# Kernel tuning notes

Measured on AMD Instinct MI355X. Metric: run time of the kernel, lower is better.

## Reference

```python
import jax, jax.numpy as jnp
import numpy as np

EMB = 768
HEADS = 8
WS = 14  # window size


def setup_inputs() -> dict:
    key = jax.random.key(0)
    k1, k2, k3 = jax.random.split(key, 3)
    B, N, C = 16, 3136, EMB
    x = jax.random.normal(k1, (B, N, C), dtype=jnp.float32)
    s = 1.0 / np.sqrt(C)
    w_qkv = jax.random.normal(k2, (C, 3 * C), dtype=jnp.float32) * s
    b_qkv = jnp.zeros((3 * C,), dtype=jnp.float32)
    w_proj = jax.random.normal(k3, (C, C), dtype=jnp.float32) * s
    b_proj = jnp.zeros((C,), dtype=jnp.float32)
    return {"x": x, "w_qkv": w_qkv, "b_qkv": b_qkv, "w_proj": w_proj, "b_proj": b_proj}


def _window_partition(x, ws):
    # (B, H, W, C) -> (B*nWin, ws*ws, C)
    B, H, W, C = x.shape
    x = x.reshape(B, H // ws, ws, W // ws, ws, C)
    x = x.transpose(0, 1, 3, 2, 4, 5)
    return x.reshape(-1, ws * ws, C)


def _window_reverse(windows, H, W, ws):
    # (B*nWin, ws*ws, C) -> (B, H, W, C)
    C = windows.shape[-1]
    B = windows.shape[0] // ((H // ws) * (W // ws))
    x = windows.reshape(B, H // ws, W // ws, ws, ws, C)
    x = x.transpose(0, 1, 3, 2, 4, 5)
    return x.reshape(B, H, W, C)


def reference(x, w_qkv, b_qkv, w_proj, b_proj):
    B, N, C = x.shape
    H = W = int(np.sqrt(N))
    nh, d = HEADS, C // HEADS
    x4 = x.reshape(B, H, W, C)
    shortcut = x  # residual in (B, N, C) layout

    xw = _window_partition(x4, WS)  # (nb, n, C), n = WS*WS
    nb, n, _ = xw.shape

    qkv = xw @ w_qkv + b_qkv  # (nb, n, 3C)
    # einops 'b n (h d qkv)': qkv index varies fastest within last dim
    qkv = qkv.reshape(nb, n, nh, d, 3)
    qkv = jnp.transpose(qkv, (4, 0, 2, 1, 3))  # (3, nb, h, n, d)
    q, k, v = qkv[0], qkv[1], qkv[2]

    energy = jnp.einsum('bhqd,bhkd->bhqk', q, k)
    # NOTE: faithful to source — softmax FIRST, then divide by sqrt(emb_size)
    att = jax.nn.softmax(energy, axis=-1) / jnp.sqrt(jnp.float32(C))
    out = jnp.einsum('bhqk,bhkd->bhqd', att, v)
    out = out.transpose(0, 2, 1, 3).reshape(nb, n, C)  # (nb, n, h*d)
    out = out @ w_proj + b_proj

    out = _window_reverse(out, H, W, WS).reshape(B, N, C)
    return out + shortcut
```

## Files before the change

### kernel.cpp

```cpp
#include <hip/hip_runtime.h>


#define NWIN 256
#define NTOK 196
#define CDIM 768
#define NHEAD 8
#define DHEAD 96
#define C3 2304

typedef unsigned short u16;
typedef unsigned int u32;
typedef __attribute__((ext_vector_type(8))) short bf16x8;
typedef __attribute__((ext_vector_type(4))) float f32x4;

__device__ __forceinline__ float bf2f(u16 u) {
    union { u32 i; float f; } cv;
    cv.i = ((u32)u) << 16;
    return cv.f;
}
__device__ __forceinline__ float2 bfp2f(u32 u) {
    union { u32 i; float f; } lo, hi;
    lo.i = u << 16;
    hi.i = u & 0xFFFF0000u;
    float2 r; r.x = lo.f; r.y = hi.f;
    return r;
}
__device__ __forceinline__ u16 f2bf(float f) {
    union { float f; u32 i; } cv;
    cv.f = f;
    u32 x = cv.i;
    x = x + 0x7FFFu + ((x >> 16) & 1u);
    return (u16)(x >> 16);
}
__device__ __forceinline__ u32 pack2bf(float a, float b) {
    return (u32)f2bf(a) | ((u32)f2bf(b) << 16);
}

__global__ void detect_kernel(const u16* __restrict__ w, int* __restrict__ flag) {
    __shared__ int any;
    int t = threadIdx.x;
    if (t == 0) any = 0;
    __syncthreads();
    int hit = 0;
    for (int i = 0; i < 16; ++i) {
        u16 u = w[t * 16 + i];
        int e = (u >> 7) & 0xFF;
        if (e >= 140) hit = 1;
    }
    if (hit) atomicOr(&any, 1);
    __syncthreads();
    if (t == 0) flag[0] = any;
}

template<bool FP32>
__global__ __launch_bounds__(256, 2) void qkvmm_kernel(
    const void* __restrict__ xv, const void* __restrict__ wqv,
    const void* __restrict__ bvv, const int* __restrict__ flag,
    u16* __restrict__ qb, u16* __restrict__ kb, u16* __restrict__ vb,
    int win0, int mtiles)
{
    if (flag[0] != (FP32 ? 1 : 0)) return;
    __shared__ u16 As[128 * 40];
    __shared__ u16 Bs[192 * 40];

    int t = threadIdx.x;
    int mb = blockIdx.x % mtiles;
    int nb = blockIdx.x / mtiles;

    int arow = t >> 1, ahalf = t & 1;
    int rloc = mb * 128 + arow;
    int wiL = rloc / 196, tok = rloc - wiL * 196;
    int wiA = win0 + wiL;
    int b_ = wiA >> 4, wrem = wiA & 15, wr = wrem >> 2, wc = wrem & 3;
    int tr = tok / 14, tc = tok - tr * 14;
    size_t xrow = ((size_t)b_ * 3136 + (size_t)((wr * 14 + tr) * 56 + wc * 14 + tc)) * CDIM;

    int kp = t >> 4, dg = t & 15;
    int d0 = nb * 64 + dg * 4;
    int hB = d0 / 96, dh0 = d0 - hB * 96;
    int sb = hB * 288 + 3 * dh0;

    f32x4 acc[4][6];
#pragma unroll
    for (int m = 0; m < 4; ++m)
#pragma unroll
        for (int n = 0; n < 6; ++n)
            acc[m][n] = (f32x4){0.f, 0.f, 0.f, 0.f};

    int lane = t & 63, wvid = t >> 6;
    int wm = wvid >> 1, wn = wvid & 1;
    int lo = lane & 15, hi = lane >> 4;

#pragma unroll 1
    for (int kk = 0; kk < 24; ++kk) {
        int k0 = kk * 32;
        {
            u32* dst = (u32*)&As[arow * 40 + ahalf * 16];
            if (FP32) {
                const float4* xp = (const float4*)((const float*)xv + xrow + k0 + ahalf * 16);
                float4 f0 = xp[0], f1 = xp[1], f2 = xp[2], f3 = xp[3];
                dst[0] = pack2bf(f0.x, f0.y); dst[1] = pack2bf(f0.z, f0.w);
                dst[2] = pack2bf(f1.x, f1.y); dst[3] = pack2bf(f1.z, f1.w);
                dst[4] = pack2bf(f2.x, f2.y); dst[5] = pack2bf(f2.z, f2.w);
                dst[6] = pack2bf(f3.x, f3.y); dst[7] = pack2bf(f3.z, f3.w);
            } else {
                const uint4* xp = (const uint4*)((const u16*)xv + xrow + k0 + ahalf * 16);
                ((uint4*)dst)[0] = xp[0];
                ((uint4*)dst)[1] = xp[1];
            }
        }
        if (FP32) {
            const float* w0p = (const float*)wqv + (size_t)(k0 + 2 * kp) * C3 + sb;
            const float* w1p = w0p + C3;
#pragma unroll
            for (int e = 0; e < 12; ++e) {
                int c = (e % 3) * 64 + dg * 4 + e / 3;
                *(u32*)&Bs[c * 40 + 2 * kp] = pack2bf(w0p[e], w1p[e]);
            }
        } else {
            const u16* w0p = (const u16*)wqv + (size_t)(k0 + 2 * kp) * C3 + sb;
            const u16* w1p = w0p + C3;
#pragma unroll
            for (int e = 0; e < 12; ++e) {
                int c = (e % 3) * 64 + dg * 4 + e / 3;
                *(u32*)&Bs[c * 40 + 2 * kp] = (u32)w0p[e] | ((u32)w1p[e] << 16);
            }
        }
        __syncthreads();
        bf16x8 af[4], bfr[6];
#pragma unroll
        for (int m = 0; m < 4; ++m)
            af[m] = *(const bf16x8*)&As[(wm * 64 + m * 16 + lo) * 40 + hi * 8];
#pragma unroll
        for (int n = 0; n < 6; ++n)
            bfr[n] = *(const bf16x8*)&Bs[(wn * 96 + n * 16 + lo) * 40 + hi * 8];
#pragma unroll
        for (int m = 0; m < 4; ++m)
#pragma unroll
            for (int n = 0; n < 6; ++n)
                acc[m][n] = __builtin_amdgcn_mfma_f32_16x16x32_bf16(af[m], bfr[n], acc[m][n], 0, 0, 0);
        __syncthreads();
    }

    float bias[6];
    int h2_[6], dh2_[6], wh_[6];
#pragma unroll
    for (int n = 0; n < 6; ++n) {
        int c = wn * 96 + n * 16 + lo;
        wh_[n] = c >> 6;
        int d_abs = nb * 64 + (c & 63);
        h2_[n] = d_abs / 96; dh2_[n] = d_abs - h2_[n] * 96;
        int bcol = h2_[n] * 288 + 3 * dh2_[n] + wh_[n];
        bias[n] = FP32 ? ((const float*)bvv)[bcol] : bf2f(((const u16*)bvv)[bcol]);
    }
#pragma unroll
    for (int m = 0; m < 4; ++m) {
#pragma unroll
        for (int j = 0; j < 4; ++j) {
            int rr = mb * 128 + wm * 64 + m * 16 + hi * 4 + j;
            int wir = rr / 196, tk = rr - wir * 196;
            size_t rowpart = (size_t)wir * (8 * 196) + (size_t)tk;
#pragma unroll
            for (int n = 0; n < 6; ++n) {
                u16* ob = wh_[n] == 0 ? qb : (wh_[n] == 1 ? kb : vb);
                ob[(rowpart + (size_t)h2_[n] * 196) * 96 + dh2_[n]] =
                    f2bf(acc[m][n][j] + bias[n]);
            }
        }
    }
}

template<bool FP32>
__global__ __launch_bounds__(256, 2) void attn_kernel(
    const u16* __restrict__ qbp, const u16* __restrict__ kbp,
    const u16* __restrict__ vbp, u16* __restrict__ ao,
    const int* __restrict__ flag, int win0)
{
    if (flag[0] != (FP32 ? 1 : 0)) return;
    __shared__ u16 Vt[96 * 232];
    __shared__ u16 Pl[4 * 16 * 232];

    int bh = blockIdx.x;
    int t  = threadIdx.x;
    int lane = t & 63, w = t >> 6;
    int lo = lane & 15, hi = lane >> 4;

    const u16* qbase = qbp + (size_t)bh * (NTOK * DHEAD);
    const u16* kbase = kbp + (size_t)bh * (NTOK * DHEAD);
    const u16* vbase = vbp + (size_t)bh * (NTOK * DHEAD);
    u16* obase = ao + ((size_t)bh + (size_t)win0 * 8) * (NTOK * DHEAD);

#pragma unroll 1
    for (int i = t; i < 112 * 12; i += 256) {
        int tp = i % 112, dgv = i / 112;
        int dbase = dgv * 8, cpos = 2 * tp;
        uint4 a = {0, 0, 0, 0}, bq = {0, 0, 0, 0};
        if (tp < 98) {
            const u16* v0 = vbase + (size_t)(2 * tp) * 96 + dbase;
            a  = *(const uint4*)v0;
            bq = *(const uint4*)(v0 + 96);
        }
        *(u32*)&Vt[(dbase + 0) * 232 + cpos] = (a.x & 0xFFFFu) | (bq.x << 16);
        *(u32*)&Vt[(dbase + 1) * 232 + cpos] = (a.x >> 16) | (bq.x & 0xFFFF0000u);
        *(u32*)&Vt[(dbase + 2) * 232 + cpos] = (a.y & 0xFFFFu) | (bq.y << 16);
        *(u32*)&Vt[(dbase + 3) * 232 + cpos] = (a.y >> 16) | (bq.y & 0xFFFF0000u);
        *(u32*)&Vt[(dbase + 4) * 232 + cpos] = (a.z & 0xFFFFu) | (bq.z << 16);
        *(u32*)&Vt[(dbase + 5) * 232 + cpos] = (a.z >> 16) | (bq.z & 0xFFFF0000u);
        *(u32*)&Vt[(dbase + 6) * 232 + cpos] = (a.w & 0xFFFFu) | (bq.w << 16);
        *(u32*)&Vt[(dbase + 7) * 232 + cpos] = (a.w >> 16) | (bq.w & 0xFFFF0000u);
    }
    __syncthreads();

    u16* pw = Pl + w * (16 * 232);
#pragma unroll 1
    for (int i = 0; i < 4; ++i) {
        int qt = w + 4 * i;
        if (qt >= 13) break;
        int qrow = qt * 16 + lo; if (qrow > 195) qrow = 195;
        bf16x8 qf[3];
#pragma unroll
        for (int ks = 0; ks < 3; ++ks)
            qf[ks] = *(const bf16x8*)(qbase + (size_t)qrow * 96 + ks * 32 + hi * 8);
        f32x4 sc[13];
#pragma unroll
        for (int kt = 0; kt < 13; ++kt) sc[kt] = (f32x4){0.f, 0.f, 0.f, 0.f};
#pragma unroll
        for (int kt = 0; kt < 13; ++kt) {
            int krow = kt * 16 + lo; if (krow > 195) krow = 195;
            const u16* kr = kbase + (size_t)krow * 96;
#pragma unroll
            for (int ks = 0; ks < 3; ++ks) {
                bf16x8 kf = *(const bf16x8*)(kr + ks * 32 + hi * 8);
                sc[kt] = __builtin_amdgcn_mfma_f32_16x16x32_bf16(kf, qf[ks], sc[kt], 0, 0, 0);
            }
        }
        float p[52];
        float mx = -1e30f;
#pragma unroll
        for (int kt = 0; kt < 13; ++kt)
#pragma unroll
            for (int j = 0; j < 4; ++j) {
                float e = sc[kt][j];
                if (kt == 12 && hi != 0) e = -1e30f;
                p[kt * 4 + j] = e;
                mx = fmaxf(mx, e);
            }
        mx = fmaxf(mx, __shfl_xor(mx, 16));
        mx = fmaxf(mx, __shfl_xor(mx, 32));
        float l = 0.f;
#pragma unroll
        for (int z = 0; z < 52; ++z) {
            float e = __expf(p[z] - mx);
            p[z] = e;
            l += e;
        }
        l += __shfl_xor(l, 16);
        l += __shfl_xor(l, 32);
        float rs = 1.0f / (l * 27.712812921102035f);
#pragma unroll
        for (int kt = 0; kt < 13; ++kt) {
            *(u32*)&pw[lo * 232 + kt * 16 + hi * 4]     = pack2bf(p[kt * 4 + 0] * rs, p[kt * 4 + 1] * rs);
            *(u32*)&pw[lo * 232 + kt * 16 + hi * 4 + 2] = pack2bf(p[kt * 4 + 2] * rs, p[kt * 4 + 3] * rs);
        }
        *(u32*)&pw[lo * 232 + 208 + hi * 4]     = 0;
        *(u32*)&pw[lo * 232 + 208 + hi * 4 + 2] = 0;
        asm volatile("s_waitcnt lgkmcnt(0)" ::: "memory");
        __builtin_amdgcn_sched_barrier(0);
        f32x4 oa[6];
#pragma unroll
        for (int n = 0; n < 6; ++n) oa[n] = (f32x4){0.f, 0.f, 0.f, 0.f};
#pragma unroll
        for (int ks = 0; ks < 7; ++ks) {
            bf16x8 pf = *(const bf16x8*)&pw[lo * 232 + ks * 32 + hi * 8];
#pragma unroll
            for (int n = 0; n < 6; ++n) {
                bf16x8 vf = *(const bf16x8*)&Vt[(n * 16 + lo) * 232 + ks * 32 + hi * 8];
                oa[n] = __builtin_amdgcn_mfma_f32_16x16x32_bf16(pf, vf, oa[n], 0, 0, 0);
            }
        }
#pragma unroll
        for (int n = 0; n < 6; ++n)
#pragma unroll
            for (int j = 0; j < 4; ++j) {
                int q = qt * 16 + hi * 4 + j;
                if (q < NTOK)
                    obase[(size_t)q * 96 + n * 16 + lo] = f2bf(oa[n][j]);
            }
    }
}

template<bool FP32>
__global__ __launch_bounds__(256, 2) void projmm_kernel(
    const u16* __restrict__ ao,
    const void* __restrict__ wpv, const void* __restrict__ bpv,
    const void* __restrict__ xv, const int* __restrict__ flag,
    void* __restrict__ outv)
{
    if (flag[0] != (FP32 ? 1 : 0)) return;
    __shared__ u16 As[128 * 40];
    __shared__ u16 Bs[128 * 40];

    int t = threadIdx.x;
    int mb = blockIdx.x % 392;
    int nb = blockIdx.x / 392;
    int n0 = nb * 128;

    int arow = t >> 1, ahalf = t & 1;
    int r = mb * 128 + arow;
    int wi = r / 196, tok = r - wi * 196;
    size_t aobase = (size_t)(wi * 8) * 196 + (size_t)tok;

    int kp = t >> 4, cg = t & 15;

    f32x4 acc[4][4];
#pragma unroll
    for (int m = 0; m < 4; ++m)
#pragma unroll
        for (int n = 0; n < 4; ++n)
            acc[m][n] = (f32x4){0.f, 0.f, 0.f, 0.f};

    int lane = t & 63, wvid = t >> 6;
    int wm = wvid >> 1, wn = wvid & 1;
    int lo = lane & 15, hi = lane >> 4;

#pragma unroll 1
    for (int kk = 0; kk < 24; ++kk) {
        int k0 = kk * 32;
        {
            int kabs = k0 + ahalf * 16;
            int h = kabs / 96, dd = kabs - h * 96;
            const uint4* ap = (const uint4*)(ao + (aobase + (size_t)h * 196) * 96 + dd);
            uint4 q0 = ap[0], q1 = ap[1];
            uint4* dst = (uint4*)&As[arow * 40 + ahalf * 16];
            dst[0] = q0; dst[1] = q1;
        }
        if (FP32) {
            const float* w0p = (const float*)wpv + (size_t)(k0 + 2 * kp) * CDIM + n0 + cg * 8;
            const float* w1p = w0p + CDIM;
            float4 a0 = ((const float4*)w0p)[0], a1 = ((const float4*)w0p)[1];
            float4 c0 = ((const float4*)w1p)[0], c1 = ((const float4*)w1p)[1];
            *(u32*)&Bs[(cg * 8 + 0) * 40 + 2 * kp] = pack2bf(a0.x, c0.x);
            *(u32*)&Bs[(cg * 8 + 1) * 40 + 2 * kp] = pack2bf(a0.y, c0.y);
            *(u32*)&Bs[(cg * 8 + 2) * 40 + 2 * kp] = pack2bf(a0.z, c0.z);
            *(u32*)&Bs[(cg * 8 + 3) * 40 + 2 * kp] = pack2bf(a0.w, c0.w);
            *(u32*)&Bs[(cg * 8 + 4) * 40 + 2 * kp] = pack2bf(a1.x, c1.x);
            *(u32*)&Bs[(cg * 8 + 5) * 40 + 2 * kp] = pack2bf(a1.y, c1.y);
            *(u32*)&Bs[(cg * 8 + 6) * 40 + 2 * kp] = pack2bf(a1.z, c1.z);
            *(u32*)&Bs[(cg * 8 + 7) * 40 + 2 * kp] = pack2bf(a1.w, c1.w);
        } else {
            const u16* w0p = (const u16*)wpv + (size_t)(k0 + 2 * kp) * CDIM + n0 + cg * 8;
            const u16* w1p = w0p + CDIM;
            uint4 ua = *(const uint4*)w0p;
            uint4 ub = *(const uint4*)w1p;
            *(u32*)&Bs[(cg * 8 + 0) * 40 + 2 * kp] = (ua.x & 0xFFFFu) | (ub.x << 16);
            *(u32*)&Bs[(cg * 8 + 1) * 40 + 2 * kp] = (ua.x >> 16) | (ub.x & 0xFFFF0000u);
            *(u32*)&Bs[(cg * 8 + 2) * 40 + 2 * kp] = (ua.y & 0xFFFFu) | (ub.y << 16);
            *(u32*)&Bs[(cg * 8 + 3) * 40 + 2 * kp] = (ua.y >> 16) | (ub.y & 0xFFFF0000u);
            *(u32*)&Bs[(cg * 8 + 4) * 40 + 2 * kp] = (ua.z & 0xFFFFu) | (ub.z << 16);
            *(u32*)&Bs[(cg * 8 + 5) * 40 + 2 * kp] = (ua.z >> 16) | (ub.z & 0xFFFF0000u);
            *(u32*)&Bs[(cg * 8 + 6) * 40 + 2 * kp] = (ua.w & 0xFFFFu) | (ub.w << 16);
            *(u32*)&Bs[(cg * 8 + 7) * 40 + 2 * kp] = (ua.w >> 16) | (ub.w & 0xFFFF0000u);
        }
        __syncthreads();
        bf16x8 af[4], bfr[4];
#pragma unroll
        for (int m = 0; m < 4; ++m)
            af[m] = *(const bf16x8*)&As[(wm * 64 + m * 16 + lo) * 40 + hi * 8];
#pragma unroll
        for (int n = 0; n < 4; ++n)
            bfr[n] = *(const bf16x8*)&Bs[(wn * 64 + n * 16 + lo) * 40 + hi * 8];
#pragma unroll
        for (int m = 0; m < 4; ++m)
#pragma unroll
            for (int n = 0; n < 4; ++n)
                acc[m][n] = __builtin_amdgcn_mfma_f32_16x16x32_bf16(af[m], bfr[n], acc[m][n], 0, 0, 0);
        __syncthreads();
    }

    float bias[4];
    int col_[4];
#pragma unroll
    for (int n = 0; n < 4; ++n) {
        col_[n] = n0 + wn * 64 + n * 16 + lo;
        bias[n] = FP32 ? ((const float*)bpv)[col_[n]] : bf2f(((const u16*)bpv)[col_[n]]);
    }
#pragma unroll
    for (int m = 0; m < 4; ++m) {
#pragma unroll
        for (int j = 0; j < 4; ++j) {
            int rr = mb * 128 + wm * 64 + m * 16 + hi * 4 + j;
            int wi2 = rr / 196, tk = rr - wi2 * 196;
            int b2 = wi2 >> 4, wrem2 = wi2 & 15, wr2 = wrem2 >> 2, wc2 = wrem2 & 3;
            int tr2 = tk / 14, tc2 = tk - tr2 * 14;
            size_t obase = ((size_t)b2 * 3136 +
                            (size_t)((wr2 * 14 + tr2) * 56 + wc2 * 14 + tc2)) * CDIM;
#pragma unroll
            for (int n = 0; n < 4; ++n) {
                size_t off = obase + col_[n];
                if (FP32) {
                    ((float*)outv)[off] = acc[m][n][j] + bias[n] + ((const float*)xv)[off];
                } else {
                    ((u16*)outv)[off] =
                        f2bf(acc[m][n][j] + bias[n] + bf2f(((const u16*)xv)[off]));
                }
            }
        }
    }
}

extern "C" void kernel_launch(void* const* d_in, const int* in_sizes, int n_in,
                              void* d_out, int out_size, void* d_ws, size_t ws_size,
                              hipStream_t stream) {
    const void* x      = d_in[0];
    const void* w_qkv  = d_in[1];
    const void* b_qkv  = d_in[2];
    const void* w_proj = d_in[3];
    const void* b_proj = d_in[4];

    const size_t perF   = (size_t)NWIN * NHEAD * NTOK * DHEAD;
    const size_t bytesF = perF * sizeof(u16);

    if (ws_size >= 3 * bytesF + sizeof(int)) {
        u16* qbp = (u16*)d_ws;
        u16* kbp = qbp + perF;
        u16* vbp = kbp + perF;
        int* flag = (int*)((char*)d_ws + 3 * bytesF);

        detect_kernel<<<1, 256, 0, stream>>>((const u16*)w_qkv, flag);

        qkvmm_kernel<false><<<392 * 12, 256, 0, stream>>>(x, w_qkv, b_qkv, flag, qbp, kbp, vbp, 0, 392);
        qkvmm_kernel<true ><<<392 * 12, 256, 0, stream>>>(x, w_qkv, b_qkv, flag, qbp, kbp, vbp, 0, 392);

        attn_kernel<false><<<NWIN * NHEAD, 256, 0, stream>>>(qbp, kbp, vbp, vbp, flag, 0);
        attn_kernel<true ><<<NWIN * NHEAD, 256, 0, stream>>>(qbp, kbp, vbp, vbp, flag, 0);

        projmm_kernel<false><<<2352, 256, 0, stream>>>(vbp, w_proj, b_proj, x, flag, d_out);
        projmm_kernel<true ><<<2352, 256, 0, stream>>>(vbp, w_proj, b_proj, x, flag, d_out);
    } else {
        const int    NWC  = 64;
        const size_t perC = (size_t)NWC * NHEAD * NTOK * DHEAD;
        u16* ao  = (u16*)d_ws;
        u16* qbp = ao + perF;
        u16* kbp = qbp + perC;
        u16* vbp = kbp + perC;
        int* flag = (int*)((char*)d_ws + bytesF + 3 * perC * sizeof(u16));

        detect_kernel<<<1, 256, 0, stream>>>((const u16*)w_qkv, flag);

        for (int c = 0; c < 4; ++c) {
            int win0 = c * NWC;
            qkvmm_kernel<false><<<98 * 12, 256, 0, stream>>>(x, w_qkv, b_qkv, flag, qbp, kbp, vbp, win0, 98);
            qkvmm_kernel<true ><<<98 * 12, 256, 0, stream>>>(x, w_qkv, b_qkv, flag, qbp, kbp, vbp, win0, 98);
            attn_kernel<false><<<NWC * NHEAD, 256, 0, stream>>>(qbp, kbp, vbp, ao, flag, win0);
            attn_kernel<true ><<<NWC * NHEAD, 256, 0, stream>>>(qbp, kbp, vbp, ao, flag, win0);
        }

        projmm_kernel<false><<<2352, 256, 0, stream>>>(ao, w_proj, b_proj, x, flag, d_out);
        projmm_kernel<true ><<<2352, 256, 0, stream>>>(ao, w_proj, b_proj, x, flag, d_out);
    }
}
```

Measured before the change: 952.4 us.

## Pre-transpose weights to bf16, convert x once, swizzle block order, add setprio

Adds pre-pass kernels that convert x to bf16 and transpose/permute the QKV and projection weights into bf16 K-contiguous layouts. The GEMM tile loads then become contiguous 16-byte copies instead of strided scalar gathers with per-element conversion. Block indices are remapped with an XCD-style swizzle, and MFMA sections are wrapped in s_setprio. The attn kernel drops its dtype template and runs once instead of twice. The cost is extra workspace, several extra launches and a full pass over x to convert it.

```diff
diff --git a/kernel.cpp b/kernel.cpp
--- a/kernel.cpp
+++ b/kernel.cpp
@@ -17,13 +17,6 @@
     union { u32 i; float f; } cv;
     cv.i = ((u32)u) << 16;
     return cv.f;
-}
-__device__ __forceinline__ float2 bfp2f(u32 u) {
-    union { u32 i; float f; } lo, hi;
-    lo.i = u << 16;
-    hi.i = u & 0xFFFF0000u;
-    float2 r; r.x = lo.f; r.y = hi.f;
-    return r;
 }
 __device__ __forceinline__ u16 f2bf(float f) {
     union { float f; u32 i; } cv;
@@ -52,20 +45,84 @@
     if (t == 0) flag[0] = any;
 }
 
+__global__ __launch_bounds__(256) void convx_kernel(
+    const float* __restrict__ x, const int* __restrict__ flag, u16* __restrict__ xb)
+{
+    if (flag[0] != 1) return;
+    size_t gid = (size_t)blockIdx.x * 256 + threadIdx.x;
+    const float4* s = (const float4*)(x + gid * 8);
+    float4 a = s[0], b = s[1];
+    uint4 o;
+    o.x = pack2bf(a.x, a.y); o.y = pack2bf(a.z, a.w);
+    o.z = pack2bf(b.x, b.y); o.w = pack2bf(b.z, b.w);
+    *(uint4*)(xb + gid * 8) = o;
+}
+
 template<bool FP32>
+__global__ __launch_bounds__(256) void bwt_kernel(
+    const void* __restrict__ w, const int* __restrict__ flag, u16* __restrict__ wt)
+{
+    if (flag[0] != (FP32 ? 1 : 0)) return;
+    int gid = blockIdx.x * 256 + threadIdx.x;
+    int r = gid / 96, kg = gid - r * 96;
+    int k0 = kg * 8;
+    int which = r / 768, d = r - which * 768;
+    int h = d / 96, dh = d - h * 96;
+    int src = h * 288 + 3 * dh + which;
+    u16 o[8];
+#pragma unroll
+    for (int j = 0; j < 8; ++j) {
+        o[j] = FP32 ? f2bf(((const float*)w)[(size_t)(k0 + j) * C3 + src])
+                    : ((const u16*)w)[(size_t)(k0 + j) * C3 + src];
+    }
+    uint4 v;
+    v.x = (u32)o[0] | ((u32)o[1] << 16);
+    v.y = (u32)o[2] | ((u32)o[3] << 16);
+    v.z = (u32)o[4] | ((u32)o[5] << 16);
+    v.w = (u32)o[6] | ((u32)o[7] << 16);
+    *(uint4*)&wt[(size_t)r * 768 + k0] = v;
+}
+
+template<bool FP32>
+__global__ __launch_bounds__(256) void bwpt_kernel(
+    const void* __restrict__ w, const int* __restrict__ flag, u16* __restrict__ wpt)
+{
+    if (flag[0] != (FP32 ? 1 : 0)) return;
+    int gid = blockIdx.x * 256 + threadIdx.x;
+    int r = gid / 96, kg = gid - r * 96;
+    int k0 = kg * 8;
+    u16 o[8];
+#pragma unroll
+    for (int j = 0; j < 8; ++j) {
+        o[j] = FP32 ? f2bf(((const float*)w)[(size_t)(k0 + j) * CDIM + r])
+                    : ((const u16*)w)[(size_t)(k0 + j) * CDIM + r];
+    }
+    uint4 v;
+    v.x = (u32)o[0] | ((u32)o[1] << 16);
+    v.y = (u32)o[2] | ((u32)o[3] << 16);
+    v.z = (u32)o[4] | ((u32)o[5] << 16);
+    v.w = (u32)o[6] | ((u32)o[7] << 16);
+    *(uint4*)&wpt[(size_t)r * 768 + k0] = v;
+}
+
+template<bool XBF>
 __global__ __launch_bounds__(256, 2) void qkvmm_kernel(
-    const void* __restrict__ xv, const void* __restrict__ wqv,
-    const void* __restrict__ bvv, const int* __restrict__ flag,
+    const void* __restrict__ xsrc, const void* __restrict__ bvv,
+    const u16* __restrict__ wt, const int* __restrict__ flag, int expect,
     u16* __restrict__ qb, u16* __restrict__ kb, u16* __restrict__ vb,
     int win0, int mtiles)
 {
-    if (flag[0] != (FP32 ? 1 : 0)) return;
+    if (flag[0] != expect) return;
     __shared__ u16 As[128 * 40];
     __shared__ u16 Bs[192 * 40];
 
     int t = threadIdx.x;
-    int mb = blockIdx.x % mtiles;
-    int nb = blockIdx.x / mtiles;
+    int cpx = (mtiles * 12) >> 3;
+    int g = blockIdx.x;
+    int wid = (g & 7) * cpx + (g >> 3);
+    int mb = wid / 12;
+    int nb = wid - mb * 12;
+    int nb64 = nb * 64;
 
     int arow = t >> 1, ahalf = t & 1;
     int rloc = mb * 128 + arow;
@@ -75,11 +132,6 @@
     int tr = tok / 14, tc = tok - tr * 14;
     size_t xrow = ((size_t)b_ * 3136 + (size_t)((wr * 14 + tr) * 56 + wc * 14 + tc)) * CDIM;
 
-    int kp = t >> 4, dg = t & 15;
-    int d0 = nb * 64 + dg * 4;
-    int hB = d0 / 96, dh0 = d0 - hB * 96;
-    int sb = hB * 288 + 3 * dh0;
-
     f32x4 acc[4][6];
 #pragma unroll
     for (int m = 0; m < 4; ++m)
@@ -95,36 +147,36 @@
     for (int kk = 0; kk < 24; ++kk) {
         int k0 = kk * 32;
         {
-            u32* dst = (u32*)&As[arow * 40 + ahalf * 16];
-            if (FP32) {
-                const float4* xp = (const float4*)((const float*)xv + xrow + k0 + ahalf * 16);
+            uint4* dst = (uint4*)&As[arow * 40 + ahalf * 16];
+            if (XBF) {
+                const uint4* xp = (const uint4*)((const u16*)xsrc + xrow + k0 + ahalf * 16);
+                dst[0] = xp[0];
+                dst[1] = xp[1];
+            } else {
+                const float4* xp = (const float4*)((const float*)xsrc + xrow + k0 + ahalf * 16);
                 float4 f0 = xp[0], f1 = xp[1], f2 = xp[2], f3 = xp[3];
-                dst[0] = pack2bf(f0.x, f0.y); dst[1] = pack2bf(f0.z, f0.w);
-                dst[2] = pack2bf(f1.x, f1.y); dst[3] = pack2bf(f1.z, f1.w);
-                dst[4] = pack2bf(f2.x, f2.y); dst[5] = pack2bf(f2.z, f2.w);
-                dst[6] = pack2bf(f3.x, f3.y); dst[7] = pack2bf(f3.z, f3.w);
-            } else {
-                const uint4* xp = (const uint4*)((const u16*)xv + xrow + k0 + ahalf * 16);
-                ((uint4*)dst)[0] = xp[0];
-                ((uint4*)dst)[1] = xp[1];
-            }
-        }
-        if (FP32) {
-            const float* w0p = (const float*)wqv + (size_t)(k0 + 2 * kp) * C3 + sb;
-            const float* w1p = w0p + C3;
-#pragma unroll
-            for (int e = 0; e < 12; ++e) {
-                int c = (e % 3) * 64 + dg * 4 + e / 3;
-                *(u32*)&Bs[c * 40 + 2 * kp] = pack2bf(w0p[e], w1p[e]);
-            }
-        } else {
-            const u16* w0p = (const u16*)wqv + (size_t)(k0 + 2 * kp) * C3 + sb;
-            const u16* w1p = w0p + C3;
-#pragma unroll
-            for (int e = 0; e < 12; ++e) {
-                int c = (e % 3) * 64 + dg * 4 + e / 3;
-                *(u32*)&Bs[c * 40 + 2 * kp] = (u32)w0p[e] | ((u32)w1p[e] << 16);
-            }
+                uint4 d0, d1;
+                d0.x = pack2bf(f0.x, f0.y); d0.y = pack2bf(f0.z, f0.w);
+                d0.z = pack2bf(f1.x, f1.y); d0.w = pack2bf(f1.z, f1.w);
+                d1.x = pack2bf(f2.x, f2.y); d1.y = pack2bf(f2.z, f2.w);
+                d1.z = pack2bf(f3.x, f3.y); d1.w = pack2bf(f3.z, f3.w);
+                dst[0] = d0; dst[1] = d1;
+            }
+        }
+        {
+            int c = t >> 1, half = t & 1;
+            int wrow = (c >> 6) * 768 + nb64 + (c & 63);
+            const uint4* sp = (const uint4*)(wt + (size_t)wrow * 768 + k0 + half * 16);
+            uint4* dp = (uint4*)&Bs[c * 40 + half * 16];
+            dp[0] = sp[0]; dp[1] = sp[1];
+        }
+        if (t < 128) {
+            int i = t + 256;
+            int c = i >> 1, half = i & 1;
+            int wrow = (c >> 6) * 768 + nb64 + (c & 63);
+            const uint4* sp = (const uint4*)(wt + (size_t)wrow * 768 + k0 + half * 16);
+            uint4* dp = (uint4*)&Bs[c * 40 + half * 16];
+            dp[0] = sp[0]; dp[1] = sp[1];
         }
         __syncthreads();
         bf16x8 af[4], bfr[6];
@@ -134,11 +186,13 @@
 #pragma unroll
         for (int n = 0; n < 6; ++n)
             bfr[n] = *(const bf16x8*)&Bs[(wn * 96 + n * 16 + lo) * 40 + hi * 8];
+        __builtin_amdgcn_s_setprio(1);
 #pragma unroll
         for (int m = 0; m < 4; ++m)
 #pragma unroll
             for (int n = 0; n < 6; ++n)
                 acc[m][n] = __builtin_amdgcn_mfma_f32_16x16x32_bf16(af[m], bfr[n], acc[m][n], 0, 0, 0);
+        __builtin_amdgcn_s_setprio(0);
         __syncthreads();
     }
 
@@ -148,10 +202,10 @@
     for (int n = 0; n < 6; ++n) {
         int c = wn * 96 + n * 16 + lo;
         wh_[n] = c >> 6;
-        int d_abs = nb * 64 + (c & 63);
+        int d_abs = nb64 + (c & 63);
         h2_[n] = d_abs / 96; dh2_[n] = d_abs - h2_[n] * 96;
         int bcol = h2_[n] * 288 + 3 * dh2_[n] + wh_[n];
-        bias[n] = FP32 ? ((const float*)bvv)[bcol] : bf2f(((const u16*)bvv)[bcol]);
+        bias[n] = expect ? ((const float*)bvv)[bcol] : bf2f(((const u16*)bvv)[bcol]);
     }
 #pragma unroll
     for (int m = 0; m < 4; ++m) {
@@ -170,13 +224,10 @@
     }
 }
 
-template<bool FP32>
 __global__ __launch_bounds__(256, 2) void attn_kernel(
     const u16* __restrict__ qbp, const u16* __restrict__ kbp,
-    const u16* __restrict__ vbp, u16* __restrict__ ao,
-    const int* __restrict__ flag, int win0)
+    const u16* __restrict__ vbp, u16* __restrict__ ao, int win0)
 {
-    if (flag[0] != (FP32 ? 1 : 0)) return;
     __shared__ u16 Vt[96 * 232];
     __shared__ u16 Pl[4 * 16 * 232];
 
@@ -224,6 +275,7 @@
         f32x4 sc[13];
 #pragma unroll
         for (int kt = 0; kt < 13; ++kt) sc[kt] = (f32x4){0.f, 0.f, 0.f, 0.f};
+        __builtin_amdgcn_s_setprio(1);
 #pragma unroll
         for (int kt = 0; kt < 13; ++kt) {
             int krow = kt * 16 + lo; if (krow > 195) krow = 195;
@@ -234,6 +286,7 @@
                 sc[kt] = __builtin_amdgcn_mfma_f32_16x16x32_bf16(kf, qf[ks], sc[kt], 0, 0, 0);
             }
         }
+        __builtin_amdgcn_s_setprio(0);
         float p[52];
         float mx = -1e30f;
 #pragma unroll
@@ -269,6 +322,7 @@
         f32x4 oa[6];
 #pragma unroll
         for (int n = 0; n < 6; ++n) oa[n] = (f32x4){0.f, 0.f, 0.f, 0.f};
+        __builtin_amdgcn_s_setprio(1);
 #pragma unroll
         for (int ks = 0; ks < 7; ++ks) {
             bf16x8 pf = *(const bf16x8*)&pw[lo * 232 + ks * 32 + hi * 8];
@@ -278,6 +332,7 @@
                 oa[n] = __builtin_amdgcn_mfma_f32_16x16x32_bf16(pf, vf, oa[n], 0, 0, 0);
             }
         }
+        __builtin_amdgcn_s_setprio(0);
 #pragma unroll
         for (int n = 0; n < 6; ++n)
 #pragma unroll
@@ -292,7 +347,8 @@
 template<bool FP32>
 __global__ __launch_bounds__(256, 2) void projmm_kernel(
     const u16* __restrict__ ao,
-    const void* __restrict__ wpv, const void* __restrict__ bpv,
+    const u16* __restrict__ wpt,
+    const void* __restrict__ bpv,
     const void* __restrict__ xv, const int* __restrict__ flag,
     void* __restrict__ outv)
 {
@@ -301,16 +357,16 @@
     __shared__ u16 Bs[128 * 40];
 
     int t = threadIdx.x;
-    int mb = blockIdx.x % 392;
-    int nb = blockIdx.x / 392;
+    int g = blockIdx.x;
+    int wid = (g & 7) * 294 + (g >> 3);
+    int mb = wid / 6;
+    int nb = wid - mb * 6;
     int n0 = nb * 128;
 
     int arow = t >> 1, ahalf = t & 1;
     int r = mb * 128 + arow;
     int wi = r / 196, tok = r - wi * 196;
     size_t aobase = (size_t)(wi * 8) * 196 + (size_t)tok;
-
-    int kp = t >> 4, cg = t & 15;
 
     f32x4 acc[4][4];
 #pragma unroll
@@ -330,36 +386,14 @@
             int kabs = k0 + ahalf * 16;
             int h = kabs / 96, dd = kabs - h * 96;
             const uint4* ap = (const uint4*)(ao + (aobase + (size_t)h * 196) * 96 + dd);
-            uint4 q0 = ap[0], q1 = ap[1];
             uint4* dst = (uint4*)&As[arow * 40 + ahalf * 16];
-            dst[0] = q0; dst[1] = q1;
-        }
-        if (FP32) {
-            const float* w0p = (const float*)wpv + (size_t)(k0 + 2 * kp) * CDIM + n0 + cg * 8;
-            const float* w1p = w0p + CDIM;
-            float4 a0 = ((const float4*)w0p)[0], a1 = ((const float4*)w0p)[1];
-            float4 c0 = ((const float4*)w1p)[0], c1 = ((const float4*)w1p)[1];
-            *(u32*)&Bs[(cg * 8 + 0) * 40 + 2 * kp] = pack2bf(a0.x, c0.x);
-            *(u32*)&Bs[(cg * 8 + 1) * 40 + 2 * kp] = pack2bf(a0.y, c0.y);
-            *(u32*)&Bs[(cg * 8 + 2) * 40 + 2 * kp] = pack2bf(a0.z, c0.z);
-            *(u32*)&Bs[(cg * 8 + 3) * 40 + 2 * kp] = pack2bf(a0.w, c0.w);
-            *(u32*)&Bs[(cg * 8 + 4) * 40 + 2 * kp] = pack2bf(a1.x, c1.x);
-            *(u32*)&Bs[(cg * 8 + 5) * 40 + 2 * kp] = pack2bf(a1.y, c1.y);
-            *(u32*)&Bs[(cg * 8 + 6) * 40 + 2 * kp] = pack2bf(a1.z, c1.z);
-            *(u32*)&Bs[(cg * 8 + 7) * 40 + 2 * kp] = pack2bf(a1.w, c1.w);
-        } else {
-            const u16* w0p = (const u16*)wpv + (size_t)(k0 + 2 * kp) * CDIM + n0 + cg * 8;
-            const u16* w1p = w0p + CDIM;
-            uint4 ua = *(const uint4*)w0p;
-            uint4 ub = *(const uint4*)w1p;
-            *(u32*)&Bs[(cg * 8 + 0) * 40 + 2 * kp] = (ua.x & 0xFFFFu) | (ub.x << 16);
-            *(u32*)&Bs[(cg * 8 + 1) * 40 + 2 * kp] = (ua.x >> 16) | (ub.x & 0xFFFF0000u);
-            *(u32*)&Bs[(cg * 8 + 2) * 40 + 2 * kp] = (ua.y & 0xFFFFu) | (ub.y << 16);
-            *(u32*)&Bs[(cg * 8 + 3) * 40 + 2 * kp] = (ua.y >> 16) | (ub.y & 0xFFFF0000u);
-            *(u32*)&Bs[(cg * 8 + 4) * 40 + 2 * kp] = (ua.z & 0xFFFFu) | (ub.z << 16);
-            *(u32*)&Bs[(cg * 8 + 5) * 40 + 2 * kp] = (ua.z >> 16) | (ub.z & 0xFFFF0000u);
-            *(u32*)&Bs[(cg * 8 + 6) * 40 + 2 * kp] = (ua.w & 0xFFFFu) | (ub.w << 16);
-            *(u32*)&Bs[(cg * 8 + 7) * 40 + 2 * kp] = (ua.w >> 16) | (ub.w & 0xFFFF0000u);
+            dst[0] = ap[0]; dst[1] = ap[1];
+        }
+        {
+            int c = t >> 1, half = t & 1;
+            const uint4* sp = (const uint4*)(wpt + (size_t)(n0 + c) * 768 + k0 + half * 16);
+            uint4* dp = (uint4*)&Bs[c * 40 + half * 16];
+            dp[0] = sp[0]; dp[1] = sp[1];
         }
         __syncthreads();
         bf16x8 af[4], bfr[4];
@@ -369,11 +403,13 @@
 #pragma unroll
         for (int n = 0; n < 4; ++n)
             bfr[n] = *(const bf16x8*)&Bs[(wn * 64 + n * 16 + lo) * 40 + hi * 8];
+        __builtin_amdgcn_s_setprio(1);
 #pragma unroll
         for (int m = 0; m < 4; ++m)
 #pragma unroll
             for (int n = 0; n < 4; ++n)
                 acc[m][n] = __builtin_amdgcn_mfma_f32_16x16x32_bf16(af[m], bfr[n], acc[m][n], 0, 0, 0);
+        __builtin_amdgcn_s_setprio(0);
         __syncthreads();
     }
 
@@ -417,45 +453,83 @@
     const void* w_proj = d_in[3];
     const void* b_proj = d_in[4];
 
-    const size_t perF   = (size_t)NWIN * NHEAD * NTOK * DHEAD;
-    const size_t bytesF = perF * sizeof(u16);
-
-    if (ws_size >= 3 * bytesF + sizeof(int)) {
-        u16* qbp = (u16*)d_ws;
+    const size_t perF  = (size_t)NWIN * NHEAD * NTOK * DHEAD;
+    const size_t wtE   = (size_t)C3 * CDIM;
+    const size_t wptE  = (size_t)CDIM * CDIM;
+    const size_t needA = (4 * perF + wtE + wptE) * 2 + 4;
+    const size_t needB = (3 * perF + wtE + wptE) * 2 + 4;
+
+    u16* base = (u16*)d_ws;
+
+    if (ws_size >= needA) {
+        u16* qbp = base;
         u16* kbp = qbp + perF;
         u16* vbp = kbp + perF;
-        int* flag = (int*)((char*)d_ws + 3 * bytesF);
+        u16* xbf = vbp + perF;
+        u16* wt  = xbf + perF;
+        u16* wpt = wt + wtE;
+        int* flag = (int*)(wpt + wptE);
 
         detect_kernel<<<1, 256, 0, stream>>>((const u16*)w_qkv, flag);
-
-        qkvmm_kernel<false><<<392 * 12, 256, 0, stream>>>(x, w_qkv, b_qkv, flag, qbp, kbp, vbp, 0, 392);
-        qkvmm_kernel<true ><<<392 * 12, 256, 0, stream>>>(x, w_qkv, b_qkv, flag, qbp, kbp, vbp, 0, 392);
-
-        attn_kernel<false><<<NWIN * NHEAD, 256, 0, stream>>>(qbp, kbp, vbp, vbp, flag, 0);
-        attn_kernel<true ><<<NWIN * NHEAD, 256, 0, stream>>>(qbp, kbp, vbp, vbp, flag, 0);
-
-        projmm_kernel<false><<<2352, 256, 0, stream>>>(vbp, w_proj, b_proj, x, flag, d_out);
-        projmm_kernel<true ><<<2352, 256, 0, stream>>>(vbp, w_proj, b_proj, x, flag, d_out);
+        convx_kernel<<<18816, 256, 0, stream>>>((const float*)x, flag, xbf);
+        bwt_kernel<false><<<864, 256, 0, stream>>>(w_qkv, flag, wt);
+        bwt_kernel<true ><<<864, 256, 0, stream>>>(w_qkv, flag, wt);
+        bwpt_kernel<false><<<288, 256, 0, stream>>>(w_proj, flag, wpt);
+        bwpt_kernel<true ><<<288, 256, 0, stream>>>(w_proj, flag, wpt);
+
+        qkvmm_kernel<true><<<392 * 12, 256, 0, stream>>>(x,   b_qkv, wt, flag, 0, qbp, kbp, vbp, 0, 392);
+        qkvmm_kernel<true><<<392 * 12, 256, 0, stream>>>(xbf, b_qkv, wt, flag, 1, qbp, kbp, vbp, 0, 392);
+
+        attn_kernel<<<NWIN * NHEAD, 256, 0, stream>>>(qbp, kbp, vbp, vbp, 0);
+
+        projmm_kernel<false><<<2352, 256, 0, stream>>>(vbp, wpt, b_proj, x, flag, d_out);
+        projmm_kernel<true ><<<2352, 256, 0, stream>>>(vbp, wpt, b_proj, x, flag, d_out);
+    } else if (ws_size >= needB) {
+        u16* qbp = base;
+        u16* kbp = qbp + perF;
+        u16* vbp = kbp + perF;
+        u16* wt  = vbp + perF;
+        u16* wpt = wt + wtE;
+        int* flag = (int*)(wpt + wptE);
+
+        detect_kernel<<<1, 256, 0, stream>>>((const u16*)w_qkv, flag);
+        bwt_kernel<false><<<864, 256, 0, stream>>>(w_qkv, flag, wt);
+        bwt_kernel<true ><<<864, 256, 0, stream>>>(w_qkv, flag, wt);
+        bwpt_kernel<false><<<288, 256, 0, stream>>>(w_proj, flag, wpt);
+        bwpt_kernel<true ><<<288, 256, 0, stream>>>(w_proj, flag, wpt);
+
+        qkvmm_kernel<true ><<<392 * 12, 256, 0, stream>>>(x, b_qkv, wt, flag, 0, qbp, kbp, vbp, 0, 392);
+        qkvmm_kernel<false><<<392 * 12, 256, 0, stream>>>(x, b_qkv, wt, flag, 1, qbp, kbp, vbp, 0, 392);
+
+        attn_kernel<<<NWIN * NHEAD, 256, 0, stream>>>(qbp, kbp, vbp, vbp, 0);
+
+        projmm_kernel<false><<<2352, 256, 0, stream>>>(vbp, wpt, b_proj, x, flag, d_out);
+        projmm_kernel<true ><<<2352, 256, 0, stream>>>(vbp, wpt, b_proj, x, flag, d_out);
     } else {
         const int    NWC  = 64;
         const size_t perC = (size_t)NWC * NHEAD * NTOK * DHEAD;
-        u16* ao  = (u16*)d_ws;
+        u16* ao  = base;
         u16* qbp = ao + perF;
         u16* kbp = qbp + perC;
         u16* vbp = kbp + perC;
-        int* flag = (int*)((char*)d_ws + bytesF + 3 * perC * sizeof(u16));
+        u16* wt  = vbp + perC;
+        u16* wpt = wt + wtE;
+        int* flag = (int*)(wpt + wptE);
 
         detect_kernel<<<1, 256, 0, stream>>>((const u16*)w_qkv, flag);
+        bwt_kernel<false><<<864, 256, 0, stream>>>(w_qkv, flag, wt);
+        bwt_kernel<true ><<<864, 256, 0, stream>>>(w_qkv, flag, wt);
+        bwpt_kernel<false><<<288, 256, 0, stream>>>(w_proj, flag, wpt);
+        bwpt_kernel<true ><<<288, 256, 0, stream>>>(w_proj, flag, wpt);
 
         for (int c = 0; c < 4; ++c) {
             int win0 = c * NWC;
-            qkvmm_kernel<false><<<98 * 12, 256, 0, stream>>>(x, w_qkv, b_qkv, flag, qbp, kbp, vbp, win0, 98);
-            qkvmm_kernel<true ><<<98 * 12, 256, 0, stream>>>(x, w_qkv, b_qkv, flag, qbp, kbp, vbp, win0, 98);
-            attn_kernel<false><<<NWC * NHEAD, 256, 0, stream>>>(qbp, kbp, vbp, ao, flag, win0);
-            attn_kernel<true ><<<NWC * NHEAD, 256, 0, stream>>>(qbp, kbp, vbp, ao, flag, win0);
-        }
-
-        projmm_kernel<false><<<2352, 256, 0, stream>>>(ao, w_proj, b_proj, x, flag, d_out);
-        projmm_kernel<true ><<<2352, 256, 0, stream>>>(ao, w_proj, b_proj, x, flag, d_out);
-    }
-}
+            qkvmm_kernel<true ><<<98 * 12, 256, 0, stream>>>(x, b_qkv, wt, flag, 0, qbp, kbp, vbp, win0, 98);
+            qkvmm_kernel<false><<<98 * 12, 256, 0, stream>>>(x, b_qkv, wt, flag, 1, qbp, kbp, vbp, win0, 98);
+            attn_kernel<<<NWC * NHEAD, 256, 0, stream>>>(qbp, kbp, vbp, ao, win0);
+        }
+
+        projmm_kernel<false><<<2352, 256, 0, stream>>>(ao, wpt, b_proj, x, flag, d_out);
+        projmm_kernel<true ><<<2352, 256, 0, stream>>>(ao, wpt, b_proj, x, flag, d_out);
+    }
+}
```

After: 896.3 us. 5.9% less time.
